# Performance work log

Measured on AMD Instinct MI355X. Metric: run time of the kernel, lower is better.

The kernel has to match this reference:

```python
import jax, jax.numpy as jnp
import numpy as np

N = 8192      # total nodes
B = 8         # graphs in batch
L = 1024      # nodes per graph (max_len)
E = 262144    # edges (before self loops)
IN = 64       # in_channels
H = 8         # heads
C = 32        # hidden_channels (per-head out dim)
D = H * C     # 256, d_model
DFF = 2048    # transformer FFN dim (torch default)
NEG = -1e9


def setup_inputs() -> dict:
    key = jax.random.key(0)
    ks = jax.random.split(key, 24)
    def p(i, shape):
        return jax.random.normal(ks[i], shape, jnp.float32) * 0.02
    x = jax.random.normal(ks[0], (N, IN), jnp.float32)
    src = jax.random.randint(ks[1], (E,), 0, N)
    dst = (src // L) * L + jax.random.randint(ks[2], (E,), 0, L)  # keep edges within a graph
    edge_index = jnp.stack([src, dst]).astype(jnp.int32)
    batch = (jnp.arange(N) // L).astype(jnp.int32)
    return dict(
        x=x, edge_index=edge_index, batch=batch,
        gat_W0=p(3, (D, IN)), gat_W12=p(4, (2, D, D)),
        gat_att_src=p(5, (3, H, C)), gat_att_dst=p(6, (3, H, C)), gat_bias=p(7, (3, D)),
        tf_qkv_w=p(8, (2, 3 * D, D)), tf_qkv_b=p(9, (2, 3 * D)),
        tf_out_w=p(10, (2, D, D)), tf_out_b=p(11, (2, D)),
        tf_ln1_w=jnp.ones((2, D)), tf_ln1_b=jnp.zeros((2, D)),
        tf_ln2_w=jnp.ones((2, D)), tf_ln2_b=jnp.zeros((2, D)),
        tf_ff1_w=p(12, (2, DFF, D)), tf_ff1_b=p(13, (2, DFF)),
        tf_ff2_w=p(14, (2, D, DFF)), tf_ff2_b=p(15, (2, D)),
        pred_w=p(16, (3, D)), pred_b=p(17, (3,)),
    )


def _gat(x, src, dst, W, att_s, att_d, bias):
    # PyG GATConv, concat=True, add_self_loops (appended in caller), eval (no dropout)
    h = (x @ W.T).reshape(-1, H, C)                       # [N,H,C]
    a_s = (h * att_s).sum(-1)                             # [N,H]
    a_d = (h * att_d).sum(-1)
    e = jax.nn.leaky_relu(a_s[src] + a_d[dst], 0.2)       # [E+N,H]
    m = jax.ops.segment_max(e, dst, num_segments=N)       # per-dst softmax
    e = jnp.exp(e - m[dst])
    s = jax.ops.segment_sum(e, dst, num_segments=N)
    alpha = e / s[dst]
    out = jax.ops.segment_sum(h[src] * alpha[..., None], dst, num_segments=N)
    return out.reshape(-1, D) + bias


def _ln(x, w, b):
    mu = x.mean(-1, keepdims=True)
    v = ((x - mu) ** 2).mean(-1, keepdims=True)
    return (x - mu) / jnp.sqrt(v + 1e-5) * w + b


def _tf_layer(x, mask, qkv_w, qkv_b, out_w, out_b, ln1w, ln1b, ln2w, ln2b, f1w, f1b, f2w, f2b):
    # torch TransformerEncoderLayer (post-LN, relu), key padding mask, eval mode
    qkv = x @ qkv_w.T + qkv_b                              # [B,L,3D]
    q, k, v = jnp.split(qkv, 3, -1)
    sh = lambda t: t.reshape(B, L, H, D // H)
    q, k, v = sh(q), sh(k), sh(v)
    sc = jnp.einsum('bqhd,bkhd->bhqk', q, k) * (1.0 / float(np.sqrt(D // H)))
    sc = jnp.where(mask[:, None, None, :], NEG, sc)
    a = jax.nn.softmax(sc, -1)
    o = jnp.einsum('bhqk,bkhd->bqhd', a, v).reshape(B, L, D)
    x = _ln(x + o @ out_w.T + out_b, ln1w, ln1b)
    f = jax.nn.relu(x @ f1w.T + f1b) @ f2w.T + f2b
    return _ln(x + f, ln2w, ln2b)


def reference(x, edge_index, batch, gat_W0, gat_W12, gat_att_src, gat_att_dst, gat_bias,
              tf_qkv_w, tf_qkv_b, tf_out_w, tf_out_b, tf_ln1_w, tf_ln1_b, tf_ln2_w, tf_ln2_b,
              tf_ff1_w, tf_ff1_b, tf_ff2_w, tf_ff2_b, pred_w, pred_b):
    loops = jnp.arange(N, dtype=edge_index.dtype)
    src = jnp.concatenate([edge_index[0], loops])
    dst = jnp.concatenate([edge_index[1], loops])
    h = jax.nn.relu(_gat(x, src, dst, gat_W0, gat_att_src[0], gat_att_dst[0], gat_bias[0]))
    for i in range(2):
        h = jax.nn.relu(_gat(h, src, dst, gat_W12[i], gat_att_src[i + 1], gat_att_dst[i + 1], gat_bias[i + 1]))
    # ragged -> padded [B, L, D] (vectorized scatter instead of python loop)
    seq_lens = jax.ops.segment_sum(jnp.ones(N, jnp.int32), batch, num_segments=B)
    starts = jnp.cumsum(seq_lens) - seq_lens
    pos = jnp.arange(N) - starts[batch]
    xp = jnp.zeros((B, L, D), h.dtype).at[batch, pos].set(h)
    mask = jnp.arange(L)[None, :] >= seq_lens[:, None]     # True = padded key
    for i in range(2):
        xp = _tf_layer(xp, mask, tf_qkv_w[i], tf_qkv_b[i], tf_out_w[i], tf_out_b[i],
                       tf_ln1_w[i], tf_ln1_b[i], tf_ln2_w[i], tf_ln2_b[i],
                       tf_ff1_w[i], tf_ff1_b[i], tf_ff2_w[i], tf_ff2_b[i])
    return xp @ pred_w.T + pred_b                          # [B,L,3]
```

## Files before the change

kernel.cpp:

```cpp
#include <hip/hip_runtime.h>
#include <hip/hip_bf16.h>

#define NN 8192
#define EE 262144
#define BB 8
#define LL 1024
#define HH 8
#define DD 256
#define DFFN 2048

typedef short s8v __attribute__((ext_vector_type(8)));
typedef float f32x4 __attribute__((ext_vector_type(4)));
typedef unsigned short ushort;

__device__ inline ushort f2bf(float f) {
    unsigned u = __float_as_uint(f);
    u = (u + 0x7fffu + ((u >> 16) & 1u)) >> 16;
    return (ushort)u;
}
__device__ inline float bf2f(ushort u) {
    return __uint_as_float(((unsigned)u) << 16);
}

template<bool BIAS, bool RELU, bool RES, bool WF, bool WB>
__global__ __launch_bounds__(256) void mgemm_kernel(
    const ushort* __restrict__ A, const ushort* __restrict__ W,
    const float* __restrict__ bias, const float* __restrict__ res,
    float* __restrict__ Cf, ushort* __restrict__ Cb, int M, int N, int K)
{
    __shared__ ushort As[128 * 32];
    __shared__ ushort Bs[128 * 32];
    int t = threadIdx.x;
    int l = t & 63;
    int quad = l >> 4, l15 = l & 15;
    int swz = (l15 >> 1) & 3;
    int rq = (quad ^ swz) * 8;
    int w = t >> 6;
    int wm = (w >> 1) * 64, wn = (w & 1) * 64;
    int m0 = blockIdx.x * 128, n0 = blockIdx.y * 128;

    f32x4 z = {0.f, 0.f, 0.f, 0.f};
    f32x4 acc[4][4];
#pragma unroll
    for (int i = 0; i < 4; ++i)
#pragma unroll
        for (int j = 0; j < 4; ++j) acc[i][j] = z;

    for (int k0 = 0; k0 < K; k0 += 32) {
#pragma unroll
        for (int i = 0; i < 2; ++i) {
            int chunk = i * 256 + t;
            int r = chunk >> 2, q = chunk & 3;
            int qs = (q ^ ((r >> 1) & 3)) * 8;
            __builtin_amdgcn_global_load_lds(
                (const __attribute__((address_space(1))) unsigned int*)
                    (A + (size_t)(m0 + r) * K + k0 + qs),
                (__attribute__((address_space(3))) unsigned int*)(As + chunk * 8), 16, 0, 0);
            __builtin_amdgcn_global_load_lds(
                (const __attribute__((address_space(1))) unsigned int*)
                    (W + (size_t)(n0 + r) * K + k0 + qs),
                (__attribute__((address_space(3))) unsigned int*)(Bs + chunk * 8), 16, 0, 0);
        }
        __syncthreads();
        s8v af[4], bfv[4];
#pragma unroll
        for (int i = 0; i < 4; ++i) {
            af[i]  = *(const s8v*)(As + (wm + i * 16 + l15) * 32 + rq);
            bfv[i] = *(const s8v*)(Bs + (wn + i * 16 + l15) * 32 + rq);
        }
#pragma unroll
        for (int mi = 0; mi < 4; ++mi)
#pragma unroll
            for (int ni = 0; ni < 4; ++ni)
                acc[mi][ni] = __builtin_amdgcn_mfma_f32_16x16x32_bf16(
                    af[mi], bfv[ni], acc[mi][ni], 0, 0, 0);
        __syncthreads();
    }

#pragma unroll
    for (int mi = 0; mi < 4; ++mi) {
#pragma unroll
        for (int ni = 0; ni < 4; ++ni) {
            int n = n0 + wn + ni * 16 + l15;
#pragma unroll
            for (int r = 0; r < 4; ++r) {
                int m = m0 + wm + mi * 16 + quad * 4 + r;
                float v = acc[mi][ni][r];
                if (BIAS) v += bias[n];
                if (RES)  v += res[(size_t)m * N + n];
                if (RELU) v = fmaxf(v, 0.f);
                if (WF) Cf[(size_t)m * N + n] = v;
                if (WB) Cb[(size_t)m * N + n] = f2bf(v);
            }
        }
    }
}

template<bool BIAS, bool RELU, bool RES, bool WF, bool WB, bool ASD>
__global__ __launch_bounds__(256) void mgemm64_kernel(
    const ushort* __restrict__ A, const ushort* __restrict__ W,
    const float* __restrict__ bias, const float* __restrict__ res,
    float* __restrict__ Cf, ushort* __restrict__ Cb,
    const float* __restrict__ atts, const float* __restrict__ attd,
    float* __restrict__ a_s, float* __restrict__ a_d, int M, int N, int K)
{
    __shared__ ushort As[64 * 64];
    __shared__ ushort Bs[64 * 64];
    int t = threadIdx.x;
    int l = t & 63;
    int quad = l >> 4, l15 = l & 15;
    int r7 = l15 & 7;
    int w = t >> 6;
    int wm = (w >> 1) * 32, wn = (w & 1) * 32;
    int m0 = blockIdx.x * 64, n0 = blockIdx.y * 64;

    f32x4 z = {0.f, 0.f, 0.f, 0.f};
    f32x4 acc[2][2];
#pragma unroll
    for (int i = 0; i < 2; ++i)
#pragma unroll
        for (int j = 0; j < 2; ++j) acc[i][j] = z;

    for (int k0 = 0; k0 < K; k0 += 64) {
#pragma unroll
        for (int i = 0; i < 2; ++i) {
            int chunk = i * 256 + t;
            int r = chunk >> 3, p = chunk & 7;
            int qs = (p ^ (r & 7)) * 8;
            __builtin_amdgcn_global_load_lds(
                (const __attribute__((address_space(1))) unsigned int*)
                    (A + (size_t)(m0 + r) * K + k0 + qs),
                (__attribute__((address_space(3))) unsigned int*)(As + chunk * 8), 16, 0, 0);
            __builtin_amdgcn_global_load_lds(
                (const __attribute__((address_space(1))) unsigned int*)
                    (W + (size_t)(n0 + r) * K + k0 + qs),
                (__attribute__((address_space(3))) unsigned int*)(Bs + chunk * 8), 16, 0, 0);
        }
        __syncthreads();
#pragma unroll
        for (int kk = 0; kk < 2; ++kk) {
            s8v af[2], bfv[2];
            int c = kk * 4 + quad;
            int off = (c ^ r7) * 8;
#pragma unroll
            for (int i = 0; i < 2; ++i) {
                af[i]  = *(const s8v*)(As + (wm + i * 16 + l15) * 64 + off);
                bfv[i] = *(const s8v*)(Bs + (wn + i * 16 + l15) * 64 + off);
            }
#pragma unroll
            for (int mi = 0; mi < 2; ++mi)
#pragma unroll
                for (int ni = 0; ni < 2; ++ni)
                    acc[mi][ni] = __builtin_amdgcn_mfma_f32_16x16x32_bf16(
                        af[mi], bfv[ni], acc[mi][ni], 0, 0, 0);
        }
        __syncthreads();
    }

#pragma unroll
    for (int mi = 0; mi < 2; ++mi) {
#pragma unroll
        for (int ni = 0; ni < 2; ++ni) {
            int n = n0 + wn + ni * 16 + l15;
#pragma unroll
            for (int r = 0; r < 4; ++r) {
                int m = m0 + wm + mi * 16 + quad * 4 + r;
                float v = acc[mi][ni][r];
                if (BIAS) v += bias[n];
                if (RES)  v += res[(size_t)m * N + n];
                if (RELU) v = fmaxf(v, 0.f);
                if (WF) Cf[(size_t)m * N + n] = v;
                if (WB) Cb[(size_t)m * N + n] = f2bf(v);
            }
        }
    }

    if (ASD) {
        int head = ((n0 + wn) >> 5) & 7;
        float as0 = atts[head * 32 + l15];
        float as1 = atts[head * 32 + 16 + l15];
        float ad0 = attd[head * 32 + l15];
        float ad1 = attd[head * 32 + 16 + l15];
#pragma unroll
        for (int mi = 0; mi < 2; ++mi)
#pragma unroll
            for (int r = 0; r < 4; ++r) {
                float sp = acc[mi][0][r] * as0 + acc[mi][1][r] * as1;
                float dp = acc[mi][0][r] * ad0 + acc[mi][1][r] * ad1;
#pragma unroll
                for (int off = 1; off < 16; off <<= 1) {
                    sp += __shfl_xor(sp, off);
                    dp += __shfl_xor(dp, off);
                }
                if (l15 == 0) {
                    int m = m0 + wm + mi * 16 + quad * 4 + r;
                    a_s[m * 8 + head] = sp;
                    a_d[m * 8 + head] = dp;
                }
            }
    }
}

__global__ __launch_bounds__(256) void mgemm_qkv_kernel(
    const ushort* __restrict__ A, const ushort* __restrict__ W,
    const float* __restrict__ bias,
    ushort* __restrict__ Qb, ushort* __restrict__ Kb, ushort* __restrict__ Vt,
    int M, int K)
{
    __shared__ ushort As[64 * 64];
    __shared__ ushort Bs[64 * 64];
    int t = threadIdx.x;
    int l = t & 63;
    int quad = l >> 4, l15 = l & 15;
    int r7 = l15 & 7;
    int w = t >> 6;
    int wm = (w >> 1) * 32, wn = (w & 1) * 32;
    int m0 = blockIdx.x * 64, n0 = blockIdx.y * 64;

    f32x4 z = {0.f, 0.f, 0.f, 0.f};
    f32x4 acc[2][2];
#pragma unroll
    for (int i = 0; i < 2; ++i)
#pragma unroll
        for (int j = 0; j < 2; ++j) acc[i][j] = z;

    for (int k0 = 0; k0 < K; k0 += 64) {
#pragma unroll
        for (int i = 0; i < 2; ++i) {
            int chunk = i * 256 + t;
            int r = chunk >> 3, p = chunk & 7;
            int qs = (p ^ (r & 7)) * 8;
            __builtin_amdgcn_global_load_lds(
                (const __attribute__((address_space(1))) unsigned int*)
                    (A + (size_t)(m0 + r) * K + k0 + qs),
                (__attribute__((address_space(3))) unsigned int*)(As + chunk * 8), 16, 0, 0);
            __builtin_amdgcn_global_load_lds(
                (const __attribute__((address_space(1))) unsigned int*)
                    (W + (size_t)(n0 + r) * K + k0 + qs),
                (__attribute__((address_space(3))) unsigned int*)(Bs + chunk * 8), 16, 0, 0);
        }
        __syncthreads();
#pragma unroll
        for (int kk = 0; kk < 2; ++kk) {
            s8v af[2], bfv[2];
            int c = kk * 4 + quad;
            int off = (c ^ r7) * 8;
#pragma unroll
            for (int i = 0; i < 2; ++i) {
                af[i]  = *(const s8v*)(As + (wm + i * 16 + l15) * 64 + off);
                bfv[i] = *(const s8v*)(Bs + (wn + i * 16 + l15) * 64 + off);
            }
#pragma unroll
            for (int mi = 0; mi < 2; ++mi)
#pragma unroll
                for (int ni = 0; ni < 2; ++ni)
                    acc[mi][ni] = __builtin_amdgcn_mfma_f32_16x16x32_bf16(
                        af[mi], bfv[ni], acc[mi][ni], 0, 0, 0);
        }
        __syncthreads();
    }

#pragma unroll
    for (int mi = 0; mi < 2; ++mi) {
#pragma unroll
        for (int ni = 0; ni < 2; ++ni) {
            int n = n0 + wn + ni * 16 + l15;
            int sec = n >> 8, hc = n & 255;
            int hh = hc >> 5, c = hc & 31;
            float bv = bias[n];
#pragma unroll
            for (int r = 0; r < 4; ++r) {
                int m = m0 + wm + mi * 16 + quad * 4 + r;
                float v = acc[mi][ni][r] + bv;
                int b = m >> 10, ll2 = m & 1023;
                int bh = b * 8 + hh;
                if (sec == 0)
                    Qb[(size_t)bh * 32768 + ll2 * 32 + c] = f2bf(v * 0.17677669529663687f);
                else if (sec == 1)
                    Kb[(size_t)bh * 32768 + ll2 * 32 + c] = f2bf(v);
                else
                    Vt[(size_t)bh * 32768 + c * 1024 + ll2] = f2bf(v);
            }
        }
    }
}

__global__ __launch_bounds__(256) void castall_kernel(
    const float* __restrict__ W0, const float* __restrict__ W12,
    const float* __restrict__ qkvw, const float* __restrict__ outw,
    const float* __restrict__ f1w, const float* __restrict__ f2w,
    const float* __restrict__ x,
    ushort* __restrict__ W0b, ushort* __restrict__ W12b,
    ushort* __restrict__ qkvb, ushort* __restrict__ outb,
    ushort* __restrict__ f1b, ushort* __restrict__ f2b,
    ushort* __restrict__ xb, int* __restrict__ deg)
{
    int tid = blockIdx.x * 256 + threadIdx.x;
    if (tid < 2048) *(int4*)(deg + tid * 4) = make_int4(0, 0, 0, 0);
    int e = tid * 4;
    if (e >= 3293184) return;
    const float* s; ushort* d; int off;
    if (e < 16384)        { s = W0;   d = W0b;  off = e; }
    else if (e < 147456)  { s = W12;  d = W12b; off = e - 16384; }
    else if (e < 540672)  { s = qkvw; d = qkvb; off = e - 147456; }
    else if (e < 671744)  { s = outw; d = outb; off = e - 540672; }
    else if (e < 1720320) { s = f1w;  d = f1b;  off = e - 671744; }
    else if (e < 2768896) { s = f2w;  d = f2b;  off = e - 1720320; }
    else                  { s = x;    d = xb;   off = e - 2768896; }
    float4 v = *(const float4*)(s + off);
    d[off + 0] = f2bf(v.x); d[off + 1] = f2bf(v.y);
    d[off + 2] = f2bf(v.z); d[off + 3] = f2bf(v.w);
}

__global__ void count_kernel(const int* __restrict__ ei, int* __restrict__ deg)
{
    int e = blockIdx.x * 256 + threadIdx.x;
    if (e >= EE + NN) return;
    int d = (e < EE) ? ei[EE + e] : (e - EE);
    atomicAdd(&deg[d], 1);
}

__global__ __launch_bounds__(1024) void scan_kernel(
    const int* __restrict__ deg, int* __restrict__ rowptr, int* __restrict__ cursor)
{
    __shared__ int part[1024];
    int t = threadIdx.x;
    int base = t * 8;
    int loc[8]; int s = 0;
#pragma unroll
    for (int i = 0; i < 8; ++i) { loc[i] = deg[base + i]; s += loc[i]; }
    part[t] = s;
    __syncthreads();
    for (int off = 1; off < 1024; off <<= 1) {
        int v = (t >= off) ? part[t - off] : 0;
        __syncthreads();
        part[t] += v;
        __syncthreads();
    }
    int run = (t == 0) ? 0 : part[t - 1];
#pragma unroll
    for (int i = 0; i < 8; ++i) { rowptr[base + i] = run; cursor[base + i] = run; run += loc[i]; }
    if (t == 1023) rowptr[NN] = run;
}

__global__ void scatter_kernel(const int* __restrict__ ei, int* __restrict__ cursor,
                               int* __restrict__ col)
{
    int e = blockIdx.x * 256 + threadIdx.x;
    if (e >= EE + NN) return;
    int s, d;
    if (e < EE) { s = ei[e]; d = ei[EE + e]; } else { s = e - EE; d = s; }
    int slot = atomicAdd(&cursor[d], 1);
    col[slot] = s;
}

__global__ __launch_bounds__(256) void gat_agg_kernel(
    const ushort* __restrict__ hlinb, const float* __restrict__ a_s,
    const float* __restrict__ a_d, const int* __restrict__ rowptr,
    const int* __restrict__ col, const float* __restrict__ bias,
    float* __restrict__ alpha_e,
    float* __restrict__ out, ushort* __restrict__ outb)
{
    int wid = threadIdx.x >> 6, lane = threadIdx.x & 63;
    int dst = blockIdx.x * 4 + wid;
    int start = rowptr[dst], end = rowptr[dst + 1];
    float ad[HH];
#pragma unroll
    for (int h = 0; h < HH; ++h) ad[h] = a_d[(size_t)dst * HH + h];

    float sm[HH];
#pragma unroll
    for (int h = 0; h < HH; ++h) sm[h] = 0.f;
    for (int e = start + lane; e < end; e += 64) {
        int s = col[e];
        float* al = alpha_e + (size_t)e * HH;
#pragma unroll
        for (int h = 0; h < HH; ++h) {
            float v = a_s[(size_t)s * HH + h] + ad[h];
            v = v > 0.f ? v : 0.2f * v;
            float p = __expf(v);
            sm[h] += p;
            al[h] = p;
        }
    }
#pragma unroll
    for (int h = 0; h < HH; ++h)
#pragma unroll
        for (int off = 32; off; off >>= 1) sm[h] += __shfl_xor(sm[h], off);

    int myh = lane >> 3;
    float invs = 1.f / sm[myh];
    float a0 = 0.f, a1 = 0.f, a2 = 0.f, a3 = 0.f;
    for (int e = start; e < end; ++e) {
        int s = col[e];
        float alpha = alpha_e[(size_t)e * HH + myh] * invs;
        uint2 hv = *(const uint2*)(hlinb + (size_t)s * DD + lane * 4);
        a0 += alpha * bf2f((ushort)(hv.x & 0xffff));
        a1 += alpha * bf2f((ushort)(hv.x >> 16));
        a2 += alpha * bf2f((ushort)(hv.y & 0xffff));
        a3 += alpha * bf2f((ushort)(hv.y >> 16));
    }
    float4 bv = *(const float4*)(bias + lane * 4);
    float r0 = fmaxf(a0 + bv.x, 0.f);
    float r1 = fmaxf(a1 + bv.y, 0.f);
    float r2 = fmaxf(a2 + bv.z, 0.f);
    float r3 = fmaxf(a3 + bv.w, 0.f);
    float* op = out + (size_t)dst * DD + lane * 4;
    op[0] = r0; op[1] = r1; op[2] = r2; op[3] = r3;
    ushort* ob = outb + (size_t)dst * DD + lane * 4;
    ob[0] = f2bf(r0); ob[1] = f2bf(r1); ob[2] = f2bf(r2); ob[3] = f2bf(r3);
}

__global__ __launch_bounds__(256, 2) void attn_flash_kernel(
    const ushort* __restrict__ Qb, const ushort* __restrict__ Kb,
    const ushort* __restrict__ Vt, ushort* __restrict__ outb)
{
    __shared__ ushort Ks[128 * 32];
    __shared__ ushort Vs[32 * 128];
    __shared__ ushort pw[4][32][132];

    int t = threadIdx.x;
    int w = t >> 6, lane = t & 63;
    int quad = lane >> 4, l15 = lane & 15;
    int kq = (quad ^ ((l15 >> 1) & 3)) * 8;
    int bh = blockIdx.y;
    int q0 = blockIdx.x * 128 + w * 32;
    int b = bh >> 3, h = bh & 7;

    const ushort* qbase = Qb + (size_t)bh * 32768;
    const ushort* kbase = Kb + (size_t)bh * 32768;
    const ushort* vbase = Vt + (size_t)bh * 32768;

    s8v aq0 = *(const s8v*)(qbase + (q0 + l15) * 32 + quad * 8);
    s8v aq1 = *(const s8v*)(qbase + (q0 + 16 + l15) * 32 + quad * 8);

    f32x4 z = {0.f, 0.f, 0.f, 0.f};
    f32x4 o00 = z, o01 = z, o10 = z, o11 = z;
    float lden0[4] = {0.f, 0.f, 0.f, 0.f};
    float lden1[4] = {0.f, 0.f, 0.f, 0.f};

    for (int ch = 0; ch < 8; ++ch) {
        int j0 = ch * 128;
#pragma unroll
        for (int i = 0; i < 2; ++i) {
            int idx = i * 256 + t;
            int kr = idx >> 2, kc = idx & 3;
            int kcs = (kc ^ ((kr >> 1) & 3)) * 8;
            __builtin_amdgcn_global_load_lds(
                (const __attribute__((address_space(1))) unsigned int*)
                    (kbase + (size_t)(j0 + kr) * 32 + kcs),
                (__attribute__((address_space(3))) unsigned int*)(Ks + idx * 8), 16, 0, 0);
            int vr = idx >> 4, vc = idx & 15;
            int vcs = (vc ^ (vr & 15)) * 8;
            __builtin_amdgcn_global_load_lds(
                (const __attribute__((address_space(1))) unsigned int*)
                    (vbase + (size_t)vr * 1024 + j0 + vcs),
                (__attribute__((address_space(3))) unsigned int*)(Vs + idx * 8), 16, 0, 0);
        }
        __syncthreads();

        f32x4 s0[8], s1[8];
#pragma unroll
        for (int kk = 0; kk < 8; ++kk) {
            s8v bk = *(const s8v*)(Ks + (kk * 16 + l15) * 32 + kq);
            s0[kk] = __builtin_amdgcn_mfma_f32_16x16x32_bf16(aq0, bk, z, 0, 0, 0);
            s1[kk] = __builtin_amdgcn_mfma_f32_16x16x32_bf16(aq1, bk, z, 0, 0, 0);
        }

        float cs0[4] = {0.f, 0.f, 0.f, 0.f};
        float cs1[4] = {0.f, 0.f, 0.f, 0.f};
#pragma unroll
        for (int kk = 0; kk < 8; ++kk) {
#pragma unroll
            for (int r = 0; r < 4; ++r) {
                float p0 = __expf(s0[kk][r]);
                float p1 = __expf(s1[kk][r]);
                cs0[r] += p0;
                cs1[r] += p1;
                pw[w][quad * 4 + r][kk * 16 + l15]      = f2bf(p0);
                pw[w][16 + quad * 4 + r][kk * 16 + l15] = f2bf(p1);
            }
        }
#pragma unroll
        for (int r = 0; r < 4; ++r) {
#pragma unroll
            for (int off = 1; off < 16; off <<= 1) {
                cs0[r] += __shfl_xor(cs0[r], off);
                cs1[r] += __shfl_xor(cs1[r], off);
            }
            lden0[r] += cs0[r];
            lden1[r] += cs1[r];
        }

#pragma unroll
        for (int kk = 0; kk < 4; ++kk) {
            s8v ap0 = *(const s8v*)(&pw[w][l15][kk * 32 + quad * 8]);
            s8v ap1 = *(const s8v*)(&pw[w][16 + l15][kk * 32 + quad * 8]);
            int c0 = ((kk * 4 + quad) ^ l15) * 8;
            s8v b0 = *(const s8v*)(Vs + (size_t)l15 * 128 + c0);
            s8v b1 = *(const s8v*)(Vs + (size_t)(16 + l15) * 128 + c0);
            o00 = __builtin_amdgcn_mfma_f32_16x16x32_bf16(ap0, b0, o00, 0, 0, 0);
            o01 = __builtin_amdgcn_mfma_f32_16x16x32_bf16(ap0, b1, o01, 0, 0, 0);
            o10 = __builtin_amdgcn_mfma_f32_16x16x32_bf16(ap1, b0, o10, 0, 0, 0);
            o11 = __builtin_amdgcn_mfma_f32_16x16x32_bf16(ap1, b1, o11, 0, 0, 0);
        }
        __syncthreads();
    }

#pragma unroll
    for (int r = 0; r < 4; ++r) {
        int row0 = q0 + quad * 4 + r;
        int row1 = row0 + 16;
        float i0 = 1.f / lden0[r];
        float i1 = 1.f / lden1[r];
        outb[(size_t)(b * 1024 + row0) * 256 + h * 32 + l15]      = f2bf(o00[r] * i0);
        outb[(size_t)(b * 1024 + row0) * 256 + h * 32 + 16 + l15] = f2bf(o01[r] * i0);
        outb[(size_t)(b * 1024 + row1) * 256 + h * 32 + l15]      = f2bf(o10[r] * i1);
        outb[(size_t)(b * 1024 + row1) * 256 + h * 32 + 16 + l15] = f2bf(o11[r] * i1);
    }
}

__global__ __launch_bounds__(256) void ln_kernel(
    float* __restrict__ x, const float* __restrict__ w, const float* __restrict__ b,
    ushort* __restrict__ xb)
{
    int wid = threadIdx.x >> 6, lane = threadIdx.x & 63;
    size_t row = blockIdx.x * 4 + wid;
    float4 v = *(float4*)(x + row * DD + lane * 4);
    float s = v.x + v.y + v.z + v.w;
#pragma unroll
    for (int off = 32; off; off >>= 1) s += __shfl_xor(s, off);
    float mu = s * (1.f / 256.f);
    float dx = v.x - mu, dy = v.y - mu, dz = v.z - mu, dw = v.w - mu;
    float q = dx * dx + dy * dy + dz * dz + dw * dw;
#pragma unroll
    for (int off = 32; off; off >>= 1) q += __shfl_xor(q, off);
    float rstd = rsqrtf(q * (1.f / 256.f) + 1e-5f);
    int c = lane * 4;
    float4 wv = *(const float4*)(w + c);
    float4 bv = *(const float4*)(b + c);
    float4 o;
    o.x = dx * rstd * wv.x + bv.x;
    o.y = dy * rstd * wv.y + bv.y;
    o.z = dz * rstd * wv.z + bv.z;
    o.w = dw * rstd * wv.w + bv.w;
    *(float4*)(x + row * DD + c) = o;
    ushort* ob = xb + row * DD + c;
    ob[0] = f2bf(o.x); ob[1] = f2bf(o.y); ob[2] = f2bf(o.z); ob[3] = f2bf(o.w);
}

__global__ __launch_bounds__(256) void ln_pred_kernel(
    const float* __restrict__ x, const float* __restrict__ w, const float* __restrict__ b,
    const float* __restrict__ pw, const float* __restrict__ pb,
    float* __restrict__ out)
{
    int wid = threadIdx.x >> 6, lane = threadIdx.x & 63;
    size_t row = blockIdx.x * 4 + wid;
    float4 v = *(const float4*)(x + row * DD + lane * 4);
    float s = v.x + v.y + v.z + v.w;
#pragma unroll
    for (int off = 32; off; off >>= 1) s += __shfl_xor(s, off);
    float mu = s * (1.f / 256.f);
    float dx = v.x - mu, dy = v.y - mu, dz = v.z - mu, dw = v.w - mu;
    float q = dx * dx + dy * dy + dz * dz + dw * dw;
#pragma unroll
    for (int off = 32; off; off >>= 1) q += __shfl_xor(q, off);
    float rstd = rsqrtf(q * (1.f / 256.f) + 1e-5f);
    int c = lane * 4;
    float4 wv = *(const float4*)(w + c);
    float4 bv = *(const float4*)(b + c);
    float4 o;
    o.x = dx * rstd * wv.x + bv.x;
    o.y = dy * rstd * wv.y + bv.y;
    o.z = dz * rstd * wv.z + bv.z;
    o.w = dw * rstd * wv.w + bv.w;
    float4 w0 = *(const float4*)(pw + c);
    float4 w1 = *(const float4*)(pw + DD + c);
    float4 w2 = *(const float4*)(pw + 2 * DD + c);
    float s0 = o.x * w0.x + o.y * w0.y + o.z * w0.z + o.w * w0.w;
    float s1 = o.x * w1.x + o.y * w1.y + o.z * w1.z + o.w * w1.w;
    float s2 = o.x * w2.x + o.y * w2.y + o.z * w2.z + o.w * w2.w;
#pragma unroll
    for (int off = 32; off; off >>= 1) {
        s0 += __shfl_xor(s0, off);
        s1 += __shfl_xor(s1, off);
        s2 += __shfl_xor(s2, off);
    }
    if (lane == 0) {
        out[row * 3 + 0] = s0 + pb[0];
        out[row * 3 + 1] = s1 + pb[1];
        out[row * 3 + 2] = s2 + pb[2];
    }
}

extern "C" void kernel_launch(void* const* d_in, const int* in_sizes, int n_in,
                              void* d_out, int out_size, void* d_ws, size_t ws_size,
                              hipStream_t stream)
{
    const float* x        = (const float*)d_in[0];
    const int*   ei       = (const int*)d_in[1];
    const float* gat_W0   = (const float*)d_in[3];
    const float* gat_W12  = (const float*)d_in[4];
    const float* att_src  = (const float*)d_in[5];
    const float* att_dst  = (const float*)d_in[6];
    const float* gat_bias = (const float*)d_in[7];
    const float* qkv_w    = (const float*)d_in[8];
    const float* qkv_b    = (const float*)d_in[9];
    const float* out_w    = (const float*)d_in[10];
    const float* out_b    = (const float*)d_in[11];
    const float* ln1_w    = (const float*)d_in[12];
    const float* ln1_b    = (const float*)d_in[13];
    const float* ln2_w    = (const float*)d_in[14];
    const float* ln2_b    = (const float*)d_in[15];
    const float* ff1_w    = (const float*)d_in[16];
    const float* ff1_b    = (const float*)d_in[17];
    const float* ff2_w    = (const float*)d_in[18];
    const float* ff2_b    = (const float*)d_in[19];
    const float* pred_w   = (const float*)d_in[20];
    const float* pred_b   = (const float*)d_in[21];
    float* outp = (float*)d_out;

    float* ws   = (float*)d_ws;
    float* hA   = ws;
    float* hB   = ws + 2097152;
    ushort* ffb  = (ushort*)(ws + 4194304);
    ushort* Qb   = (ushort*)(ws + 12582912);
    ushort* Kb   = (ushort*)(ws + 13631488);
    ushort* Vt   = (ushort*)(ws + 14680064);
    ushort* attnb= (ushort*)(ws + 15728640);
    ushort* lnb  = (ushort*)(ws + 16777216);
    ushort* hBb  = (ushort*)(ws + 17825792);
    ushort* xb   = (ushort*)(ws + 18874368);
    ushort* wbase= (ushort*)(ws + 19136512);
    ushort* W0b    = wbase;
    ushort* W12b   = wbase + 16384;
    ushort* qkv_wb = wbase + 147456;
    ushort* out_wb = wbase + 540672;
    ushort* ff1_wb = wbase + 671744;
    ushort* ff2_wb = wbase + 1720320;
    float* a_s  = ws + 20520960;
    float* a_d  = ws + 20586496;
    int*   iw   = (int*)(ws + 20652032);
    int*   deg    = iw;
    int*   rowptr = iw + 8192;
    int*   cursor = iw + 16392;
    int*   col    = iw + 24592;
    ushort* hAb    = (ushort*)(ws + 21000192);
    float*  alpha_e = ws + 22048768;

    castall_kernel<<<3216, 256, 0, stream>>>(
        gat_W0, gat_W12, qkv_w, out_w, ff1_w, ff2_w, x,
        W0b, W12b, qkv_wb, out_wb, ff1_wb, ff2_wb, xb, deg);

    int etot = EE + NN;
    count_kernel<<<(etot + 255) / 256, 256, 0, stream>>>(ei, deg);
    scan_kernel<<<1, 1024, 0, stream>>>(deg, rowptr, cursor);
    scatter_kernel<<<(etot + 255) / 256, 256, 0, stream>>>(ei, cursor, col);

    mgemm64_kernel<false, false, false, false, true, true><<<dim3(128, 4), 256, 0, stream>>>(
        xb, W0b, nullptr, nullptr, nullptr, hAb, att_src, att_dst, a_s, a_d, NN, DD, 64);
    gat_agg_kernel<<<2048, 256, 0, stream>>>(hAb, a_s, a_d, rowptr, col, gat_bias,
                                             alpha_e, hB, hBb);

    for (int l = 0; l < 2; ++l) {
        mgemm64_kernel<false, false, false, false, true, true><<<dim3(128, 4), 256, 0, stream>>>(
            hBb, W12b + (size_t)l * DD * DD, nullptr, nullptr, nullptr, hAb,
            att_src + (l + 1) * 256, att_dst + (l + 1) * 256, a_s, a_d, NN, DD, DD);
        gat_agg_kernel<<<2048, 256, 0, stream>>>(
            hAb, a_s, a_d, rowptr, col, gat_bias + (l + 1) * 256, alpha_e, hB, hBb);
    }

    for (int l = 0; l < 2; ++l) {
        mgemm_qkv_kernel<<<dim3(128, 12), 256, 0, stream>>>(
            hBb, qkv_wb + (size_t)l * 768 * DD, qkv_b + l * 768, Qb, Kb, Vt, NN, DD);
        attn_flash_kernel<<<dim3(8, 64), 256, 0, stream>>>(Qb, Kb, Vt, attnb);
        mgemm64_kernel<true, false, true, true, false, false><<<dim3(128, 4), 256, 0, stream>>>(
            attnb, out_wb + (size_t)l * DD * DD, out_b + l * DD, hB,
            hA, nullptr, nullptr, nullptr, nullptr, nullptr, NN, DD, DD);
        ln_kernel<<<2048, 256, 0, stream>>>(hA, ln1_w + l * DD, ln1_b + l * DD, lnb);
        mgemm_kernel<true, true, false, false, true><<<dim3(64, 16), 256, 0, stream>>>(
            lnb, ff1_wb + (size_t)l * DFFN * DD, ff1_b + l * DFFN, nullptr,
            nullptr, ffb, NN, DFFN, DD);
        mgemm64_kernel<true, false, true, true, false, false><<<dim3(128, 4), 256, 0, stream>>>(
            ffb, ff2_wb + (size_t)l * DD * DFFN, ff2_b + l * DD, hA,
            hB, nullptr, nullptr, nullptr, nullptr, nullptr, NN, DD, DFFN);
        if (l == 0) {
            ln_kernel<<<2048, 256, 0, stream>>>(hB, ln2_w + l * DD, ln2_b + l * DD, hBb);
        } else {
            ln_pred_kernel<<<2048, 256, 0, stream>>>(
                hB, ln2_w + l * DD, ln2_b + l * DD, pred_w, pred_b, outp);
        }
    }
}
```

Measured before the change: 451.7 us.

## Double-buffer K/V tiles in flash attention and widen GEMM K-tile to 64

The flash attention kernel now double-buffers its K and V shared-memory tiles. The next chunk's global-to-LDS loads are issued before computing on the current chunk, which drops one barrier per iteration and overlaps loads with MFMA work. The 128x128 GEMM kernel now stages a K-tile of 64 instead of 32 with an 8-way XOR swizzle, halving the number of barrier pairs per output tile. In exchange, LDS use doubles in both kernels, which may lower occupancy.

```diff
diff --git a/kernel.cpp b/kernel.cpp
--- a/kernel.cpp
+++ b/kernel.cpp
@@ -28,13 +28,12 @@
     const float* __restrict__ bias, const float* __restrict__ res,
     float* __restrict__ Cf, ushort* __restrict__ Cb, int M, int N, int K)
 {
-    __shared__ ushort As[128 * 32];
-    __shared__ ushort Bs[128 * 32];
+    __shared__ ushort As[128 * 64];
+    __shared__ ushort Bs[128 * 64];
     int t = threadIdx.x;
     int l = t & 63;
     int quad = l >> 4, l15 = l & 15;
-    int swz = (l15 >> 1) & 3;
-    int rq = (quad ^ swz) * 8;
+    int r7 = l15 & 7;
     int w = t >> 6;
     int wm = (w >> 1) * 64, wn = (w & 1) * 64;
     int m0 = blockIdx.x * 128, n0 = blockIdx.y * 128;
@@ -46,12 +45,12 @@
 #pragma unroll
         for (int j = 0; j < 4; ++j) acc[i][j] = z;
 
-    for (int k0 = 0; k0 < K; k0 += 32) {
-#pragma unroll
-        for (int i = 0; i < 2; ++i) {
+    for (int k0 = 0; k0 < K; k0 += 64) {
+#pragma unroll
+        for (int i = 0; i < 4; ++i) {
             int chunk = i * 256 + t;
-            int r = chunk >> 2, q = chunk & 3;
-            int qs = (q ^ ((r >> 1) & 3)) * 8;
+            int r = chunk >> 3, p = chunk & 7;
+            int qs = (p ^ (r & 7)) * 8;
             __builtin_amdgcn_global_load_lds(
                 (const __attribute__((address_space(1))) unsigned int*)
                     (A + (size_t)(m0 + r) * K + k0 + qs),
@@ -62,18 +61,22 @@
                 (__attribute__((address_space(3))) unsigned int*)(Bs + chunk * 8), 16, 0, 0);
         }
         __syncthreads();
-        s8v af[4], bfv[4];
-#pragma unroll
-        for (int i = 0; i < 4; ++i) {
-            af[i]  = *(const s8v*)(As + (wm + i * 16 + l15) * 32 + rq);
-            bfv[i] = *(const s8v*)(Bs + (wn + i * 16 + l15) * 32 + rq);
-        }
-#pragma unroll
-        for (int mi = 0; mi < 4; ++mi)
-#pragma unroll
-            for (int ni = 0; ni < 4; ++ni)
-                acc[mi][ni] = __builtin_amdgcn_mfma_f32_16x16x32_bf16(
-                    af[mi], bfv[ni], acc[mi][ni], 0, 0, 0);
+#pragma unroll
+        for (int kk = 0; kk < 2; ++kk) {
+            int off = ((kk * 4 + quad) ^ r7) * 8;
+            s8v af[4], bfv[4];
+#pragma unroll
+            for (int i = 0; i < 4; ++i) {
+                af[i]  = *(const s8v*)(As + (wm + i * 16 + l15) * 64 + off);
+                bfv[i] = *(const s8v*)(Bs + (wn + i * 16 + l15) * 64 + off);
+            }
+#pragma unroll
+            for (int mi = 0; mi < 4; ++mi)
+#pragma unroll
+                for (int ni = 0; ni < 4; ++ni)
+                    acc[mi][ni] = __builtin_amdgcn_mfma_f32_16x16x32_bf16(
+                        af[mi], bfv[ni], acc[mi][ni], 0, 0, 0);
+        }
         __syncthreads();
     }
 
@@ -140,8 +143,7 @@
 #pragma unroll
         for (int kk = 0; kk < 2; ++kk) {
             s8v af[2], bfv[2];
-            int c = kk * 4 + quad;
-            int off = (c ^ r7) * 8;
+            int off = ((kk * 4 + quad) ^ r7) * 8;
 #pragma unroll
             for (int i = 0; i < 2; ++i) {
                 af[i]  = *(const s8v*)(As + (wm + i * 16 + l15) * 64 + off);
@@ -243,8 +245,7 @@
 #pragma unroll
         for (int kk = 0; kk < 2; ++kk) {
             s8v af[2], bfv[2];
-            int c = kk * 4 + quad;
-            int off = (c ^ r7) * 8;
+            int off = ((kk * 4 + quad) ^ r7) * 8;
 #pragma unroll
             for (int i = 0; i < 2; ++i) {
                 af[i]  = *(const s8v*)(As + (wm + i * 16 + l15) * 64 + off);
@@ -415,8 +416,8 @@
     const ushort* __restrict__ Qb, const ushort* __restrict__ Kb,
     const ushort* __restrict__ Vt, ushort* __restrict__ outb)
 {
-    __shared__ ushort Ks[128 * 32];
-    __shared__ ushort Vs[32 * 128];
+    __shared__ ushort Ks[2][128 * 32];
+    __shared__ ushort Vs[2][32 * 128];
     __shared__ ushort pw[4][32][132];
 
     int t = threadIdx.x;
@@ -434,35 +435,48 @@
     s8v aq0 = *(const s8v*)(qbase + (q0 + l15) * 32 + quad * 8);
     s8v aq1 = *(const s8v*)(qbase + (q0 + 16 + l15) * 32 + quad * 8);
 
+    int i0 = t, i1 = 256 + t;
+    int kr0 = i0 >> 2, kcs0 = (((i0 & 3)) ^ ((kr0 >> 1) & 3)) * 8;
+    int kr1 = i1 >> 2, kcs1 = (((i1 & 3)) ^ ((kr1 >> 1) & 3)) * 8;
+    int vr0 = i0 >> 4, vcs0 = ((i0 & 15) ^ (vr0 & 15)) * 8;
+    int vr1 = i1 >> 4, vcs1 = ((i1 & 15) ^ (vr1 & 15)) * 8;
+
+#define STAGE(ch, bf)                                                          \
+    {                                                                          \
+        int j0 = (ch) * 128;                                                   \
+        __builtin_amdgcn_global_load_lds(                                      \
+            (const __attribute__((address_space(1))) unsigned int*)            \
+                (kbase + (size_t)(j0 + kr0) * 32 + kcs0),                      \
+            (__attribute__((address_space(3))) unsigned int*)(Ks[bf] + i0 * 8), 16, 0, 0); \
+        __builtin_amdgcn_global_load_lds(                                      \
+            (const __attribute__((address_space(1))) unsigned int*)            \
+                (kbase + (size_t)(j0 + kr1) * 32 + kcs1),                      \
+            (__attribute__((address_space(3))) unsigned int*)(Ks[bf] + i1 * 8), 16, 0, 0); \
+        __builtin_amdgcn_global_load_lds(                                      \
+            (const __attribute__((address_space(1))) unsigned int*)            \
+                (vbase + (size_t)vr0 * 1024 + j0 + vcs0),                      \
+            (__attribute__((address_space(3))) unsigned int*)(Vs[bf] + i0 * 8), 16, 0, 0); \
+        __builtin_amdgcn_global_load_lds(                                      \
+            (const __attribute__((address_space(1))) unsigned int*)            \
+                (vbase + (size_t)vr1 * 1024 + j0 + vcs1),                      \
+            (__attribute__((address_space(3))) unsigned int*)(Vs[bf] + i1 * 8), 16, 0, 0); \
+    }
+
     f32x4 z = {0.f, 0.f, 0.f, 0.f};
     f32x4 o00 = z, o01 = z, o10 = z, o11 = z;
     float lden0[4] = {0.f, 0.f, 0.f, 0.f};
     float lden1[4] = {0.f, 0.f, 0.f, 0.f};
 
+    STAGE(0, 0);
     for (int ch = 0; ch < 8; ++ch) {
-        int j0 = ch * 128;
-#pragma unroll
-        for (int i = 0; i < 2; ++i) {
-            int idx = i * 256 + t;
-            int kr = idx >> 2, kc = idx & 3;
-            int kcs = (kc ^ ((kr >> 1) & 3)) * 8;
-            __builtin_amdgcn_global_load_lds(
-                (const __attribute__((address_space(1))) unsigned int*)
-                    (kbase + (size_t)(j0 + kr) * 32 + kcs),
-                (__attribute__((address_space(3))) unsigned int*)(Ks + idx * 8), 16, 0, 0);
-            int vr = idx >> 4, vc = idx & 15;
-            int vcs = (vc ^ (vr & 15)) * 8;
-            __builtin_amdgcn_global_load_lds(
-                (const __attribute__((address_space(1))) unsigned int*)
-                    (vbase + (size_t)vr * 1024 + j0 + vcs),
-                (__attribute__((address_space(3))) unsigned int*)(Vs + idx * 8), 16, 0, 0);
-        }
-        __syncthreads();
+        int bf = ch & 1;
+        __syncthreads();
+        if (ch < 7) STAGE(ch + 1, bf ^ 1);
 
         f32x4 s0[8], s1[8];
 #pragma unroll
         for (int kk = 0; kk < 8; ++kk) {
-            s8v bk = *(const s8v*)(Ks + (kk * 16 + l15) * 32 + kq);
+            s8v bk = *(const s8v*)(Ks[bf] + (kk * 16 + l15) * 32 + kq);
             s0[kk] = __builtin_amdgcn_mfma_f32_16x16x32_bf16(aq0, bk, z, 0, 0, 0);
             s1[kk] = __builtin_amdgcn_mfma_f32_16x16x32_bf16(aq1, bk, z, 0, 0, 0);
         }
@@ -497,26 +511,26 @@
             s8v ap0 = *(const s8v*)(&pw[w][l15][kk * 32 + quad * 8]);
             s8v ap1 = *(const s8v*)(&pw[w][16 + l15][kk * 32 + quad * 8]);
             int c0 = ((kk * 4 + quad) ^ l15) * 8;
-            s8v b0 = *(const s8v*)(Vs + (size_t)l15 * 128 + c0);
-            s8v b1 = *(const s8v*)(Vs + (size_t)(16 + l15) * 128 + c0);
+            s8v b0 = *(const s8v*)(Vs[bf] + (size_t)l15 * 128 + c0);
+            s8v b1 = *(const s8v*)(Vs[bf] + (size_t)(16 + l15) * 128 + c0);
             o00 = __builtin_amdgcn_mfma_f32_16x16x32_bf16(ap0, b0, o00, 0, 0, 0);
             o01 = __builtin_amdgcn_mfma_f32_16x16x32_bf16(ap0, b1, o01, 0, 0, 0);
             o10 = __builtin_amdgcn_mfma_f32_16x16x32_bf16(ap1, b0, o10, 0, 0, 0);
             o11 = __builtin_amdgcn_mfma_f32_16x16x32_bf16(ap1, b1, o11, 0, 0, 0);
         }
-        __syncthreads();
-    }
+    }
+#undef STAGE
 
 #pragma unroll
     for (int r = 0; r < 4; ++r) {
         int row0 = q0 + quad * 4 + r;
         int row1 = row0 + 16;
-        float i0 = 1.f / lden0[r];
-        float i1 = 1.f / lden1[r];
-        outb[(size_t)(b * 1024 + row0) * 256 + h * 32 + l15]      = f2bf(o00[r] * i0);
-        outb[(size_t)(b * 1024 + row0) * 256 + h * 32 + 16 + l15] = f2bf(o01[r] * i0);
-        outb[(size_t)(b * 1024 + row1) * 256 + h * 32 + l15]      = f2bf(o10[r] * i1);
-        outb[(size_t)(b * 1024 + row1) * 256 + h * 32 + 16 + l15] = f2bf(o11[r] * i1);
+        float i0v = 1.f / lden0[r];
+        float i1v = 1.f / lden1[r];
+        outb[(size_t)(b * 1024 + row0) * 256 + h * 32 + l15]      = f2bf(o00[r] * i0v);
+        outb[(size_t)(b * 1024 + row0) * 256 + h * 32 + 16 + l15] = f2bf(o01[r] * i0v);
+        outb[(size_t)(b * 1024 + row1) * 256 + h * 32 + l15]      = f2bf(o10[r] * i1v);
+        outb[(size_t)(b * 1024 + row1) * 256 + h * 32 + 16 + l15] = f2bf(o11[r] * i1v);
     }
 }
 
```

Result: no change. 447.8 us (-0.9%).
